# Kernel optimization log

Measured on AMD Instinct MI355X. Metric: run time of the kernel, lower is better.

## Reference

```python
import jax, jax.numpy as jnp
import numpy as np
import math

B, T, C = 2, 2048, 1024
NH = 16
HD = C // NH

def setup_inputs() -> dict:
    key = jax.random.key(0)
    ks = jax.random.split(key, 3)
    scale = 0.02
    return {
        "x": jax.random.normal(ks[0], (B, T, C), dtype=jnp.float32),
        "Wqkv": jax.random.normal(ks[1], (C, 3 * C), dtype=jnp.float32) * scale,
        "bqkv": jnp.zeros((3 * C,), dtype=jnp.float32),
        "Wproj": jax.random.normal(ks[2], (C, C), dtype=jnp.float32) * scale,
        "bproj": jnp.zeros((C,), dtype=jnp.float32),
    }

def reference(x, Wqkv, bqkv, Wproj, bproj):
    b, t, c = x.shape
    qkv = x @ Wqkv + bqkv                      # (B,T,3C)
    qkv = qkv.reshape(b, t, 3, NH, HD)
    q = jnp.transpose(qkv[:, :, 0], (0, 2, 1, 3))  # (B,H,T,D)
    k = jnp.transpose(qkv[:, :, 1], (0, 2, 1, 3))
    v = jnp.transpose(qkv[:, :, 2], (0, 2, 1, 3))
    att = jnp.einsum('bhqd,bhkd->bhqk', q, k) / math.sqrt(HD)
    causal = jnp.tril(jnp.ones((t, t), dtype=bool))
    att = jnp.where(causal[None, None], att, jnp.float32(-jnp.inf))
    att = jax.nn.softmax(att, axis=-1)
    y = jnp.einsum('bhqk,bhkd->bhqd', att, v)  # (B,H,T,D)
    y = jnp.transpose(y, (0, 2, 1, 3)).reshape(b, t, c)
    return y @ Wproj + bproj
```

## Files before the change

### kernel.cpp

```cpp
#include <hip/hip_runtime.h>


typedef __attribute__((ext_vector_type(8))) short short8;
typedef __attribute__((ext_vector_type(4))) float f32x4;
struct ushort4_t { unsigned short x, y, z, w; };

#define MFMA16(a, b, c) __builtin_amdgcn_mfma_f32_16x16x32_bf16((a), (b), (c), 0, 0, 0)

__device__ __forceinline__ unsigned short f2bf(float f) {
  unsigned u = __builtin_bit_cast(unsigned, f);
  u += 0x7fffu + ((u >> 16) & 1u);
  return (unsigned short)(u >> 16);
}

__device__ __forceinline__ void gl2lds16(const void* g, void* l) {
  __builtin_amdgcn_global_load_lds(
      (__attribute__((address_space(1))) void*)g,
      (__attribute__((address_space(3))) void*)l,
      16, 0, 0);
}

__global__ __launch_bounds__(256) void conv_bf16(const float* __restrict__ src,
                                                 unsigned short* __restrict__ dst,
                                                 int n) {
  int i = (blockIdx.x * 256 + threadIdx.x) * 4;
  if (i >= n) return;
  float4 f = *(const float4*)(src + i);
  unsigned long long r = (unsigned long long)f2bf(f.x)
      | ((unsigned long long)f2bf(f.y) << 16)
      | ((unsigned long long)f2bf(f.z) << 32)
      | ((unsigned long long)f2bf(f.w) << 48);
  *(unsigned long long*)(dst + i) = r;
}

__global__ __launch_bounds__(256) void transpose_conv(const float* __restrict__ W,
                                                      unsigned short* __restrict__ WT,
                                                      int K, int N) {
  __shared__ float tile[64][65];
  const int n0 = blockIdx.x * 64, k0 = blockIdx.y * 64;
  const int tid = threadIdx.x;
  const int c = tid & 63, rbase = tid >> 6;
#pragma unroll
  for (int i = 0; i < 16; ++i) {
    int r = i * 4 + rbase;
    tile[r][c] = W[(size_t)(k0 + r) * N + n0 + c];
  }
  __syncthreads();
#pragma unroll
  for (int i = 0; i < 16; ++i) {
    int r = i * 4 + rbase;
    WT[(size_t)(n0 + r) * K + k0 + c] = f2bf(tile[c][r]);
  }
}

template <int EPI, int MT>
__global__ __launch_bounds__(256)
void gemm_bt(const unsigned short* __restrict__ A,
             const unsigned short* __restrict__ BT,
             const float* __restrict__ bias,
             float* __restrict__ outF,
             unsigned short* __restrict__ q_out,
             unsigned short* __restrict__ k_out,
             unsigned short* __restrict__ vT_out,
             int Ndim, int Kdim) {
  constexpr int IF = MT / 32;
  constexpr int RA = MT / 32;
  __shared__ __align__(16) unsigned short As[MT * 64];
  __shared__ __align__(16) unsigned short Bs[128 * 64];
  const int tid = threadIdx.x;
  const int wave = tid >> 6, lane = tid & 63;
  const int quad = lane >> 4, lr = lane & 15;
  const int wm = wave >> 1, wn = wave & 1;
  const int m0 = blockIdx.y * MT, n0 = blockIdx.x * 128;

  const int r_l = tid >> 3;
  const int cg = (tid & 7) ^ (r_l & 7);
  const unsigned short* gA = A + (size_t)(m0 + r_l) * Kdim + cg * 8;
  const unsigned short* gB = BT + (size_t)(n0 + r_l) * Kdim + cg * 8;
  const size_t rstep = (size_t)32 * Kdim;

  f32x4 acc[IF][4] = {};
  for (int k0 = 0; k0 < Kdim; k0 += 64) {
#pragma unroll
    for (int rd = 0; rd < RA; ++rd)
      gl2lds16(gA + k0 + rd * rstep, As + rd * 2048 + wave * 512);
#pragma unroll
    for (int rd = 0; rd < 4; ++rd)
      gl2lds16(gB + k0 + rd * rstep, Bs + rd * 2048 + wave * 512);
    __syncthreads();
#pragma unroll
    for (int s = 0; s < 2; ++s) {
      const int sw = ((s * 4 + quad) ^ (lr & 7)) * 8;
      short8 a[IF], b[4];
#pragma unroll
      for (int i = 0; i < IF; ++i)
        a[i] = *(const short8*)(As + (wm * (MT / 2) + i * 16 + lr) * 64 + sw);
#pragma unroll
      for (int j = 0; j < 4; ++j)
        b[j] = *(const short8*)(Bs + (wn * 64 + j * 16 + lr) * 64 + sw);
#pragma unroll
      for (int i = 0; i < IF; ++i)
#pragma unroll
        for (int j = 0; j < 4; ++j)
          acc[i][j] = MFMA16(a[i], b[j], acc[i][j]);
    }
    __syncthreads();
  }

  const int row_t = wm * (MT / 2) + quad * 4;
  const int col_t = wn * 64 + lr;
  if (EPI == 0) {
    const int sec = n0 >> 10;
#pragma unroll
    for (int j = 0; j < 4; ++j) {
      const int n = n0 + col_t + j * 16;
      const float bi = bias[n];
      const int nn = n & 1023, h = nn >> 6, d = nn & 63;
#pragma unroll
      for (int i = 0; i < IF; ++i) {
        const int m_base = m0 + row_t + i * 16;
        const int bb = m_base >> 11, t0 = m_base & 2047;
        const int bh = bb * 16 + h;
        if (sec == 2) {
          ushort4_t pk;
          pk.x = f2bf(acc[i][j][0] + bi);
          pk.y = f2bf(acc[i][j][1] + bi);
          pk.z = f2bf(acc[i][j][2] + bi);
          pk.w = f2bf(acc[i][j][3] + bi);
          *(ushort4_t*)(vT_out + ((size_t)bh * 64 + d) * 2048 + t0) = pk;
        } else {
          unsigned short* dst = (sec == 0 ? q_out : k_out) + (size_t)bh * 131072 + t0 * 64 + d;
#pragma unroll
          for (int r = 0; r < 4; ++r)
            dst[r * 64] = f2bf(acc[i][j][r] + bi);
        }
      }
    }
  } else {
#pragma unroll
    for (int i = 0; i < IF; ++i)
#pragma unroll
      for (int r = 0; r < 4; ++r) {
        const int m = m0 + row_t + i * 16 + r;
#pragma unroll
        for (int j = 0; j < 4; ++j) {
          const int n = n0 + col_t + j * 16;
          outF[(size_t)m * Ndim + n] = acc[i][j][r] + bias[n];
        }
      }
  }
}

__global__ __launch_bounds__(256)
void attn(const unsigned short* __restrict__ qbuf,
          const unsigned short* __restrict__ kbuf,
          const unsigned short* __restrict__ vT,
          unsigned short* __restrict__ yb) {
  __shared__ __align__(16) unsigned short Ks[2][4096];
  __shared__ __align__(16) unsigned short Vs[2][4096];
  __shared__ __align__(16) unsigned short Ps[4][2][1152];
  const int tid = threadIdx.x, wave = tid >> 6, lane = tid & 63;
  const int quad = lane >> 4, lr = lane & 15;
  const int bh = blockIdx.y;
  const int qx = 15 - (int)blockIdx.x;
  const int qb = qx * 128 + wave * 32;

  const unsigned short* qp0 = qbuf + (size_t)bh * 131072;
  const unsigned short* kp0 = kbuf + (size_t)bh * 131072;
  const unsigned short* vp0 = vT   + (size_t)bh * 131072;

  short8 aq[2][2];
#pragma unroll
  for (int g = 0; g < 2; ++g) {
    const unsigned short* qp = qp0 + (size_t)(qb + g * 16 + lr) * 64 + quad * 8;
    aq[g][0] = *(const short8*)qp;
    aq[g][1] = *(const short8*)(qp + 32);
  }

  short8 ones;
#pragma unroll
  for (int i = 0; i < 8; ++i) ones[i] = (short)0x3F80;

  const int sr = tid >> 3;
  const int scg = (tid & 7) ^ (sr & 7);
  int kvoff[4][2];
#pragma unroll
  for (int jt = 0; jt < 4; ++jt)
#pragma unroll
    for (int h = 0; h < 2; ++h)
      kvoff[jt][h] = (jt * 16 + lr) * 64 + (((quad + 4 * h) ^ (lr & 7)) << 3);

  f32x4 o[2][4] = {};
  f32x4 lacc[2] = {};
  const float C = 0.18033688f;
  const int klast = 2 * qx + 1;

  auto stage = [&](int buf, int kt) {
    const unsigned short* kg = kp0 + (size_t)(kt * 64 + sr) * 64 + scg * 8;
    const unsigned short* vg = vp0 + (size_t)sr * 2048 + kt * 64 + scg * 8;
    gl2lds16(kg,             &Ks[buf][wave * 512]);
    gl2lds16(kg + 32 * 64,   &Ks[buf][2048 + wave * 512]);
    gl2lds16(vg,             &Vs[buf][wave * 512]);
    gl2lds16(vg + 32 * 2048, &Vs[buf][2048 + wave * 512]);
  };

  stage(0, 0);
  int buf = 0;
  for (int kt = 0; kt <= klast; ++kt) {
    __syncthreads();
    if (kt < klast) stage(buf ^ 1, kt + 1);
    const int k0 = kt * 64;
    const unsigned short* Kb = Ks[buf];
    const unsigned short* Vb = Vs[buf];
    short8 bk[4][2];
#pragma unroll
    for (int jt = 0; jt < 4; ++jt) {
      bk[jt][0] = *(const short8*)(Kb + kvoff[jt][0]);
      bk[jt][1] = *(const short8*)(Kb + kvoff[jt][1]);
    }
    const bool msk = (k0 + 63) > qb;
#pragma unroll
    for (int g = 0; g < 2; ++g) {
      f32x4 s[4] = {};
#pragma unroll
      for (int jt = 0; jt < 4; ++jt) {
        s[jt] = MFMA16(aq[g][0], bk[jt][0], s[jt]);
        s[jt] = MFMA16(aq[g][1], bk[jt][1], s[jt]);
      }
      unsigned short* pw = Ps[wave][g];
      const int qr = qb + g * 16 + quad * 4;
#pragma unroll
      for (int jt = 0; jt < 4; ++jt) {
        const int key = k0 + jt * 16 + lr;
#pragma unroll
        for (int r = 0; r < 4; ++r) {
          float p = __builtin_amdgcn_exp2f(s[jt][r] * C);
          if (msk && key > qr + r) p = 0.f;
          pw[(quad * 4 + r) * 72 + jt * 16 + lr] = f2bf(p);
        }
      }
    }
    short8 bv[4][2];
#pragma unroll
    for (int jt = 0; jt < 4; ++jt) {
      bv[jt][0] = *(const short8*)(Vb + kvoff[jt][0]);
      bv[jt][1] = *(const short8*)(Vb + kvoff[jt][1]);
    }
#pragma unroll
    for (int g = 0; g < 2; ++g) {
      const unsigned short* pw = Ps[wave][g];
      const short8 ap0 = *(const short8*)(pw + lr * 72 + quad * 8);
      const short8 ap1 = *(const short8*)(pw + lr * 72 + 32 + quad * 8);
      lacc[g] = MFMA16(ap0, ones, lacc[g]);
      lacc[g] = MFMA16(ap1, ones, lacc[g]);
#pragma unroll
      for (int jt = 0; jt < 4; ++jt) {
        o[g][jt] = MFMA16(ap0, bv[jt][0], o[g][jt]);
        o[g][jt] = MFMA16(ap1, bv[jt][1], o[g][jt]);
      }
    }
    buf ^= 1;
  }

  const int b = bh >> 4, h = bh & 15;
#pragma unroll
  for (int g = 0; g < 2; ++g)
#pragma unroll
    for (int jt = 0; jt < 4; ++jt)
#pragma unroll
      for (int r = 0; r < 4; ++r) {
        const float v = o[g][jt][r] / lacc[g][r];
        const int t = qb + g * 16 + quad * 4 + r;
        yb[((size_t)b * 2048 + t) * 1024 + h * 64 + jt * 16 + lr] = f2bf(v);
      }
}

extern "C" void kernel_launch(void* const* d_in, const int* in_sizes, int n_in,
                              void* d_out, int out_size, void* d_ws, size_t ws_size,
                              hipStream_t stream) {
  const float* x     = (const float*)d_in[0];
  const float* Wqkv  = (const float*)d_in[1];
  const float* bqkv  = (const float*)d_in[2];
  const float* Wproj = (const float*)d_in[3];
  const float* bproj = (const float*)d_in[4];
  float* out = (float*)d_out;

  char* ws = (char*)d_ws;
  unsigned short* xb     = (unsigned short*)(ws);
  unsigned short* wqkvT  = (unsigned short*)(ws + 8388608);
  unsigned short* wprojT = (unsigned short*)(ws + 14680064);
  unsigned short* qbuf   = (unsigned short*)(ws + 16777216);
  unsigned short* kbuf   = (unsigned short*)(ws + 25165824);
  unsigned short* vTbuf  = (unsigned short*)(ws + 33554432);
  unsigned short* ybuf   = (unsigned short*)(ws + 41943040);

  conv_bf16<<<4096, 256, 0, stream>>>(x, xb, 4194304);
  transpose_conv<<<dim3(48, 16), 256, 0, stream>>>(Wqkv, wqkvT, 1024, 3072);
  transpose_conv<<<dim3(16, 16), 256, 0, stream>>>(Wproj, wprojT, 1024, 1024);
  gemm_bt<0, 128><<<dim3(24, 32), 256, 0, stream>>>(xb, wqkvT, bqkv, nullptr,
                                                    qbuf, kbuf, vTbuf, 3072, 1024);
  attn<<<dim3(16, 32), 256, 0, stream>>>(qbuf, kbuf, vTbuf, ybuf);
  gemm_bt<1, 64><<<dim3(8, 64), 256, 0, stream>>>(ybuf, wprojT, bproj, out,
                                                  nullptr, nullptr, nullptr, 1024, 1024);
}
```

Before: 207.8 us.

## Halve attention query tile, rotate tile order, swizzle P buffer and specialize mask

The attention kernel now gives each block 64 query rows (16 per wave) instead of 128, doubling the grid to 32x32. Tile order is rotated per head so causal work is spread across the grid. The P staging buffer uses an XOR-swizzled layout to avoid LDS bank conflicts, masking runs only on the diagonal tile, and rounding and the final division use cheaper forms. Each K/V tile is now reused across fewer query rows, which raises K/V load traffic, and the no-tie-handling bf16 rounding changes P values slightly.

```diff
diff --git a/kernel.cpp b/kernel.cpp
--- a/kernel.cpp
+++ b/kernel.cpp
@@ -11,6 +11,10 @@
   unsigned u = __builtin_bit_cast(unsigned, f);
   u += 0x7fffu + ((u >> 16) & 1u);
   return (unsigned short)(u >> 16);
+}
+
+__device__ __forceinline__ unsigned short f2bf_fast(float f) {
+  return (unsigned short)((__builtin_bit_cast(unsigned, f) + 0x8000u) >> 16);
 }
 
 __device__ __forceinline__ void gl2lds16(const void* g, void* l) {
@@ -151,31 +155,27 @@
   }
 }
 
-__global__ __launch_bounds__(256)
+__global__ __launch_bounds__(256, 4)
 void attn(const unsigned short* __restrict__ qbuf,
           const unsigned short* __restrict__ kbuf,
           const unsigned short* __restrict__ vT,
           unsigned short* __restrict__ yb) {
   __shared__ __align__(16) unsigned short Ks[2][4096];
   __shared__ __align__(16) unsigned short Vs[2][4096];
-  __shared__ __align__(16) unsigned short Ps[4][2][1152];
+  __shared__ __align__(16) unsigned short Ps[4][1024];
   const int tid = threadIdx.x, wave = tid >> 6, lane = tid & 63;
   const int quad = lane >> 4, lr = lane & 15;
   const int bh = blockIdx.y;
-  const int qx = 15 - (int)blockIdx.x;
-  const int qb = qx * 128 + wave * 32;
+  const int qt = ((int)blockIdx.x + bh) & 31;
+  const int qb = qt * 64 + wave * 16;
 
   const unsigned short* qp0 = qbuf + (size_t)bh * 131072;
   const unsigned short* kp0 = kbuf + (size_t)bh * 131072;
   const unsigned short* vp0 = vT   + (size_t)bh * 131072;
 
-  short8 aq[2][2];
-#pragma unroll
-  for (int g = 0; g < 2; ++g) {
-    const unsigned short* qp = qp0 + (size_t)(qb + g * 16 + lr) * 64 + quad * 8;
-    aq[g][0] = *(const short8*)qp;
-    aq[g][1] = *(const short8*)(qp + 32);
-  }
+  const unsigned short* qp = qp0 + (size_t)(qb + lr) * 64 + quad * 8;
+  const short8 aq0 = *(const short8*)qp;
+  const short8 aq1 = *(const short8*)(qp + 32);
 
   short8 ones;
 #pragma unroll
@@ -189,11 +189,20 @@
 #pragma unroll
     for (int h = 0; h < 2; ++h)
       kvoff[jt][h] = (jt * 16 + lr) * 64 + (((quad + 4 * h) ^ (lr & 7)) << 3);
-
-  f32x4 o[2][4] = {};
-  f32x4 lacc[2] = {};
+  int pwoff[4][4];
+#pragma unroll
+  for (int jt = 0; jt < 4; ++jt)
+#pragma unroll
+    for (int r = 0; r < 4; ++r) {
+      const int row = quad * 4 + r;
+      pwoff[jt][r] = row * 64 + (((jt * 2 + (lr >> 3)) ^ (row & 7)) << 3) + (lr & 7);
+    }
+  const int proff0 = lr * 64 + ((quad ^ (lr & 7)) << 3);
+  const int proff1 = lr * 64 + (((quad + 4) ^ (lr & 7)) << 3);
+
+  f32x4 o[4] = {};
+  f32x4 lacc = {};
   const float C = 0.18033688f;
-  const int klast = 2 * qx + 1;
 
   auto stage = [&](int buf, int kt) {
     const unsigned short* kg = kp0 + (size_t)(kt * 64 + sr) * 64 + scg * 8;
@@ -206,10 +215,10 @@
 
   stage(0, 0);
   int buf = 0;
-  for (int kt = 0; kt <= klast; ++kt) {
+  unsigned short* pw = Ps[wave];
+  for (int kt = 0; kt <= qt; ++kt) {
     __syncthreads();
-    if (kt < klast) stage(buf ^ 1, kt + 1);
-    const int k0 = kt * 64;
+    if (kt < qt) stage(buf ^ 1, kt + 1);
     const unsigned short* Kb = Ks[buf];
     const unsigned short* Vb = Vs[buf];
     short8 bk[4][2];
@@ -218,27 +227,30 @@
       bk[jt][0] = *(const short8*)(Kb + kvoff[jt][0]);
       bk[jt][1] = *(const short8*)(Kb + kvoff[jt][1]);
     }
-    const bool msk = (k0 + 63) > qb;
-#pragma unroll
-    for (int g = 0; g < 2; ++g) {
-      f32x4 s[4] = {};
+    f32x4 s[4] = {};
+#pragma unroll
+    for (int jt = 0; jt < 4; ++jt) {
+      s[jt] = MFMA16(aq0, bk[jt][0], s[jt]);
+      s[jt] = MFMA16(aq1, bk[jt][1], s[jt]);
+    }
+    if (kt == qt) {
+      const int qr = qb + quad * 4;
 #pragma unroll
       for (int jt = 0; jt < 4; ++jt) {
-        s[jt] = MFMA16(aq[g][0], bk[jt][0], s[jt]);
-        s[jt] = MFMA16(aq[g][1], bk[jt][1], s[jt]);
-      }
-      unsigned short* pw = Ps[wave][g];
-      const int qr = qb + g * 16 + quad * 4;
-#pragma unroll
-      for (int jt = 0; jt < 4; ++jt) {
-        const int key = k0 + jt * 16 + lr;
+        const int key = kt * 64 + jt * 16 + lr;
 #pragma unroll
         for (int r = 0; r < 4; ++r) {
           float p = __builtin_amdgcn_exp2f(s[jt][r] * C);
-          if (msk && key > qr + r) p = 0.f;
-          pw[(quad * 4 + r) * 72 + jt * 16 + lr] = f2bf(p);
+          if (key > qr + r) p = 0.f;
+          pw[pwoff[jt][r]] = f2bf_fast(p);
         }
       }
+    } else {
+#pragma unroll
+      for (int jt = 0; jt < 4; ++jt)
+#pragma unroll
+        for (int r = 0; r < 4; ++r)
+          pw[pwoff[jt][r]] = f2bf_fast(__builtin_amdgcn_exp2f(s[jt][r] * C));
     }
     short8 bv[4][2];
 #pragma unroll
@@ -246,33 +258,30 @@
       bv[jt][0] = *(const short8*)(Vb + kvoff[jt][0]);
       bv[jt][1] = *(const short8*)(Vb + kvoff[jt][1]);
     }
-#pragma unroll
-    for (int g = 0; g < 2; ++g) {
-      const unsigned short* pw = Ps[wave][g];
-      const short8 ap0 = *(const short8*)(pw + lr * 72 + quad * 8);
-      const short8 ap1 = *(const short8*)(pw + lr * 72 + 32 + quad * 8);
-      lacc[g] = MFMA16(ap0, ones, lacc[g]);
-      lacc[g] = MFMA16(ap1, ones, lacc[g]);
-#pragma unroll
-      for (int jt = 0; jt < 4; ++jt) {
-        o[g][jt] = MFMA16(ap0, bv[jt][0], o[g][jt]);
-        o[g][jt] = MFMA16(ap1, bv[jt][1], o[g][jt]);
-      }
+    const short8 ap0 = *(const short8*)(pw + proff0);
+    const short8 ap1 = *(const short8*)(pw + proff1);
+    lacc = MFMA16(ap0, ones, lacc);
+    lacc = MFMA16(ap1, ones, lacc);
+#pragma unroll
+    for (int jt = 0; jt < 4; ++jt) {
+      o[jt] = MFMA16(ap0, bv[jt][0], o[jt]);
+      o[jt] = MFMA16(ap1, bv[jt][1], o[jt]);
     }
     buf ^= 1;
   }
 
   const int b = bh >> 4, h = bh & 15;
-#pragma unroll
-  for (int g = 0; g < 2; ++g)
-#pragma unroll
-    for (int jt = 0; jt < 4; ++jt)
-#pragma unroll
-      for (int r = 0; r < 4; ++r) {
-        const float v = o[g][jt][r] / lacc[g][r];
-        const int t = qb + g * 16 + quad * 4 + r;
-        yb[((size_t)b * 2048 + t) * 1024 + h * 64 + jt * 16 + lr] = f2bf(v);
-      }
+  float inv[4];
+#pragma unroll
+  for (int r = 0; r < 4; ++r) inv[r] = __builtin_amdgcn_rcpf(lacc[r]);
+#pragma unroll
+  for (int jt = 0; jt < 4; ++jt)
+#pragma unroll
+    for (int r = 0; r < 4; ++r) {
+      const int t = qb + quad * 4 + r;
+      yb[((size_t)b * 2048 + t) * 1024 + h * 64 + jt * 16 + lr] =
+          f2bf(o[jt][r] * inv[r]);
+    }
 }
 
 extern "C" void kernel_launch(void* const* d_in, const int* in_sizes, int n_in,
@@ -299,7 +308,7 @@
   transpose_conv<<<dim3(16, 16), 256, 0, stream>>>(Wproj, wprojT, 1024, 1024);
   gemm_bt<0, 128><<<dim3(24, 32), 256, 0, stream>>>(xb, wqkvT, bqkv, nullptr,
                                                     qbuf, kbuf, vTbuf, 3072, 1024);
-  attn<<<dim3(16, 32), 256, 0, stream>>>(qbuf, kbuf, vTbuf, ybuf);
+  attn<<<dim3(32, 32), 256, 0, stream>>>(qbuf, kbuf, vTbuf, ybuf);
   gemm_bt<1, 64><<<dim3(8, 64), 256, 0, stream>>>(ybuf, wprojT, bproj, out,
                                                   nullptr, nullptr, nullptr, 1024, 1024);
 }
```

Result: faster. 185.6 us (-10.7%).
